# Performance work log

Measured on AMD Instinct MI355X. Metric: run time of the kernel, lower is better.

## Reference

```python
import jax, jax.numpy as jnp
import numpy as np

EMBED_DIM = 512

def setup_inputs() -> dict:
    key = jax.random.key(0)
    ks = jax.random.split(key, 8)
    B, N, M, C = 4, 4096, 4096, EMBED_DIM
    s = 1.0 / np.sqrt(C)
    return {
        "rgb_features": jax.random.normal(ks[0], (B, N, C), jnp.float32),
        "depth_features": jax.random.normal(ks[1], (B, M, C), jnp.float32),
        "Wq": jax.random.normal(ks[2], (C, C), jnp.float32) * s,
        "bq": jnp.zeros((C,), jnp.float32),
        "Wk": jax.random.normal(ks[3], (C, C), jnp.float32) * s,
        "bk": jnp.zeros((C,), jnp.float32),
        "Wv": jax.random.normal(ks[4], (C, C), jnp.float32) * s,
        "bv": jnp.zeros((C,), jnp.float32),
    }

def reference(rgb_features, depth_features, Wq, bq, Wk, bk, Wv, bv):
    C = rgb_features.shape[-1]
    scale = C ** (-0.5)
    Q = rgb_features @ Wq + bq          # [B, N, C]
    K = depth_features @ Wk + bk        # [B, M, C]
    V = depth_features @ Wv + bv        # [B, M, C]
    scores = jnp.einsum('bnc,bmc->bnm', Q, K) * scale
    attn = jax.nn.softmax(scores, axis=-1)
    return jnp.einsum('bnm,bmc->bnc', attn, V)
```

## Files before the change

kernel.cpp:

```cpp
#include <hip/hip_runtime.h>
#include <hip/hip_bf16.h>
#include <stdint.h>


typedef unsigned short u16;
typedef __attribute__((ext_vector_type(8))) short bf16x8;
typedef __attribute__((ext_vector_type(16))) float f32x16;
typedef __attribute__((ext_vector_type(4))) unsigned short u16x4;

#define GLD_LDS16(g, l)                                                        \
  __builtin_amdgcn_global_load_lds(                                            \
      (const __attribute__((address_space(1))) unsigned int*)(g),              \
      (__attribute__((address_space(3))) unsigned int*)(l), 16, 0, 0)

__device__ __forceinline__ u16 f2bf(float f) {
  unsigned x = __float_as_uint(f);
  return (u16)((x + 0x7fffu + ((x >> 16) & 1u)) >> 16);
}

template <int TM, int TN, int WC, int BIAS_MODE, bool OUT_F32, bool SCALE_EN,
          int MINW>
__global__ __launch_bounds__(256, MINW) void gemm32(
    const u16* __restrict__ A, const u16* __restrict__ Bm,
    const float* __restrict__ bias, void* __restrict__ Cv, int M, int N, int K,
    long long sAb, long long sBb, long long sCb, float scale) {
  constexpr int WROWS = TM * WC / 4;
  constexpr int WCOLS = TN / WC;
  constexpr int MSUB = WROWS / 32;
  constexpr int NSUB = WCOLS / 32;
  constexpr int CA = TM / 64;
  constexpr int CB = TN / 64;

  const int bz = blockIdx.z;
  A += (size_t)bz * sAb;
  Bm += (size_t)bz * sBb;

  const int bm = blockIdx.y * TM;
  const int bn = blockIdx.x * TN;

  __shared__ u16 As[TM * 32];
  __shared__ u16 Bs[TN * 32];

  const int tid = threadIdx.x;
  const int wave = tid >> 6;
  const int lane = tid & 63;
  const int ln31 = lane & 31;
  const int half = lane >> 5;
  const int wr = wave / WC;
  const int wc = wave % WC;

  const int rowA = lane >> 2;
  const int swz = ((lane & 3) ^ ((rowA + (rowA >> 2)) & 3)) * 8;
  const int gl = (ln31 + (ln31 >> 2)) & 3;

  f32x16 acc[MSUB][NSUB] = {};

  for (int k0 = 0; k0 < K; k0 += 32) {
    __syncthreads();
#pragma unroll
    for (int r = 0; r < CA; ++r) {
      const int ch = wave * CA + r;
      GLD_LDS16(A + (size_t)(bm + ch * 16 + rowA) * K + k0 + swz,
                As + ch * 16 * 32);
    }
#pragma unroll
    for (int r = 0; r < CB; ++r) {
      const int ch = wave * CB + r;
      GLD_LDS16(Bm + (size_t)(bn + ch * 16 + rowA) * K + k0 + swz,
                Bs + ch * 16 * 32);
    }
    __syncthreads();

#pragma unroll
    for (int kc = 0; kc < 2; ++kc) {
      const int p = ((kc * 2 + half) ^ gl) * 8;
      bf16x8 af[MSUB], bfv[NSUB];
#pragma unroll
      for (int mt = 0; mt < MSUB; ++mt)
        af[mt] = *(const bf16x8*)&As[(wr * WROWS + mt * 32 + ln31) * 32 + p];
#pragma unroll
      for (int nt = 0; nt < NSUB; ++nt)
        bfv[nt] = *(const bf16x8*)&Bs[(wc * WCOLS + nt * 32 + ln31) * 32 + p];
#pragma unroll
      for (int mt = 0; mt < MSUB; ++mt)
#pragma unroll
        for (int nt = 0; nt < NSUB; ++nt)
          acc[mt][nt] = __builtin_amdgcn_mfma_f32_32x32x16_bf16(
              af[mt], bfv[nt], acc[mt][nt], 0, 0, 0);
    }
  }

  const int crow0 = bm + wr * WROWS + 4 * half;
  const int ccol0 = bn + wc * WCOLS + ln31;
#pragma unroll
  for (int mt = 0; mt < MSUB; ++mt) {
#pragma unroll
    for (int nt = 0; nt < NSUB; ++nt) {
      const int col = ccol0 + nt * 32;
#pragma unroll
      for (int r = 0; r < 16; ++r) {
        const int row = crow0 + mt * 32 + (r & 3) + 8 * (r >> 2);
        float v = acc[mt][nt][r];
        if constexpr (SCALE_EN) v *= scale;
        if constexpr (BIAS_MODE == 1) v += bias[col];
        if constexpr (BIAS_MODE == 2) v += bias[row];
        const size_t idx = (size_t)bz * (size_t)sCb + (size_t)row * N + col;
        if constexpr (OUT_F32)
          ((float*)Cv)[idx] = v;
        else
          ((u16*)Cv)[idx] = f2bf(v);
      }
    }
  }
}

__global__ __launch_bounds__(256) void cvt_pair(const float* __restrict__ x,
                                                const float* __restrict__ y,
                                                u16* __restrict__ ox,
                                                u16* __restrict__ oy, int n4) {
  const int i = blockIdx.x * 256 + threadIdx.x;
  if (i >= n4) return;
  const float4 a = ((const float4*)x)[i];
  const float4 b = ((const float4*)y)[i];
  u16x4 oa, ob;
  oa[0] = f2bf(a.x); oa[1] = f2bf(a.y); oa[2] = f2bf(a.z); oa[3] = f2bf(a.w);
  ob[0] = f2bf(b.x); ob[1] = f2bf(b.y); ob[2] = f2bf(b.z); ob[3] = f2bf(b.w);
  ((u16x4*)ox)[i] = oa;
  ((u16x4*)oy)[i] = ob;
}

__global__ __launch_bounds__(256) void wtrans_k(const float* __restrict__ W,
                                                u16* __restrict__ WT) {
  const int tr = blockIdx.y * 64;
  const int tc = blockIdx.x * 64;
  __shared__ float T[64][65];
  const int t = threadIdx.x;
  const int r0 = t >> 4;
  const int c0 = (t & 15) * 4;
#pragma unroll
  for (int rr = 0; rr < 4; ++rr) {
    const int row = rr * 16 + r0;
    const float4 w = *(const float4*)&W[(size_t)(tr + row) * 512 + tc + c0];
    T[row][c0 + 0] = w.x; T[row][c0 + 1] = w.y;
    T[row][c0 + 2] = w.z; T[row][c0 + 3] = w.w;
  }
  __syncthreads();
#pragma unroll
  for (int rr = 0; rr < 4; ++rr) {
    const int orow = rr * 16 + r0;
    u16x4 o;
#pragma unroll
    for (int j = 0; j < 4; ++j) o[j] = f2bf(T[c0 + j][orow]);
    *(u16x4*)&WT[(size_t)(tc + orow) * 512 + tr + c0] = o;
  }
}

__global__ __launch_bounds__(256) void softmax_rows(u16* __restrict__ S,
                                                    int cols) {
  u16* p = S + (size_t)blockIdx.x * (size_t)cols;
  const int tid = threadIdx.x;
  const int lane = tid & 63;
  const int wave = tid >> 6;

  uint4 d[2];
  d[0] = ((const uint4*)p)[tid];
  d[1] = ((const uint4*)p)[tid + 256];

  float v[16];
#pragma unroll
  for (int i = 0; i < 2; ++i) {
    const unsigned* w = (const unsigned*)&d[i];
#pragma unroll
    for (int j = 0; j < 4; ++j) {
      v[i * 8 + j * 2 + 0] = __uint_as_float(w[j] << 16);
      v[i * 8 + j * 2 + 1] = __uint_as_float(w[j] & 0xffff0000u);
    }
  }

  float mx = -3.4e38f;
#pragma unroll
  for (int i = 0; i < 16; ++i) mx = fmaxf(mx, v[i]);
#pragma unroll
  for (int o = 32; o > 0; o >>= 1) mx = fmaxf(mx, __shfl_xor(mx, o, 64));

  __shared__ float red[4];
  if (lane == 0) red[wave] = mx;
  __syncthreads();
  mx = fmaxf(fmaxf(red[0], red[1]), fmaxf(red[2], red[3]));

  float s = 0.f;
#pragma unroll
  for (int i = 0; i < 16; ++i) {
    v[i] = __expf(v[i] - mx);
    s += v[i];
  }
#pragma unroll
  for (int o = 32; o > 0; o >>= 1) s += __shfl_xor(s, o, 64);
  __syncthreads();
  if (lane == 0) red[wave] = s;
  __syncthreads();
  s = (red[0] + red[1]) + (red[2] + red[3]);
  const float inv = 1.0f / s;

  uint4 o4[2];
#pragma unroll
  for (int i = 0; i < 2; ++i) {
    unsigned* w = (unsigned*)&o4[i];
#pragma unroll
    for (int j = 0; j < 4; ++j) {
      const unsigned lo = f2bf(v[i * 8 + j * 2 + 0] * inv);
      const unsigned hi = f2bf(v[i * 8 + j * 2 + 1] * inv);
      w[j] = lo | (hi << 16);
    }
  }
  ((uint4*)p)[tid] = o4[0];
  ((uint4*)p)[tid + 256] = o4[1];
}

extern "C" void kernel_launch(void* const* d_in, const int* in_sizes, int n_in,
                              void* d_out, int out_size, void* d_ws,
                              size_t ws_size, hipStream_t stream) {
  const float* rgb = (const float*)d_in[0];
  const float* dep = (const float*)d_in[1];
  const float* Wq = (const float*)d_in[2];
  const float* bq = (const float*)d_in[3];
  const float* Wk = (const float*)d_in[4];
  const float* bk = (const float*)d_in[5];
  const float* Wv = (const float*)d_in[6];
  const float* bv = (const float*)d_in[7];
  float* out = (float*)d_out;

  const int B = 4, N = 4096, M = 4096, C = 512;
  const size_t nBNC = (size_t)B * N * C;
  const float scale = 0.044194173824159216f;

  char* ws = (char*)d_ws;
  size_t off = 0;
  auto carve = [&](size_t bytes) -> void* {
    void* p = ws + off;
    off += (bytes + 255) & ~(size_t)255;
    return p;
  };
  u16* rgb_bf = (u16*)carve(nBNC * 2);
  u16* dep_bf = (u16*)carve(nBNC * 2);
  u16* WqT = (u16*)carve((size_t)C * C * 2);
  u16* WkT = (u16*)carve((size_t)C * C * 2);
  u16* WvT = (u16*)carve((size_t)C * C * 2);
  u16* Qb = (u16*)carve(nBNC * 2);
  u16* Kb = (u16*)carve(nBNC * 2);
  u16* Vt = (u16*)carve(nBNC * 2);
  const size_t base = off;
  const size_t sFull = (size_t)B * N * M * 2;
  const size_t sOne = (size_t)N * M * 2;
  const bool full = ws_size >= base + sFull;
  u16* Sb = (u16*)carve(full ? sFull : sOne);

  cvt_pair<<<8192, 256, 0, stream>>>(rgb, dep, rgb_bf, dep_bf, (int)(nBNC / 4));
  wtrans_k<<<dim3(8, 8), 256, 0, stream>>>(Wq, WqT);
  wtrans_k<<<dim3(8, 8), 256, 0, stream>>>(Wk, WkT);
  wtrans_k<<<dim3(8, 8), 256, 0, stream>>>(Wv, WvT);

  const long long strQ = (long long)N * C;
  const long long strS = (long long)N * M;
  const long long strV = (long long)C * M;

  gemm32<128, 128, 2, 1, false, false, 4><<<dim3(4, 128, 1), 256, 0, stream>>>(
      rgb_bf, WqT, bq, Qb, 16384, 512, 512, 0, 0, 0, 1.f);
  gemm32<128, 128, 2, 1, false, false, 4><<<dim3(4, 128, 1), 256, 0, stream>>>(
      dep_bf, WkT, bk, Kb, 16384, 512, 512, 0, 0, 0, 1.f);
  gemm32<128, 128, 2, 2, false, false, 4><<<dim3(32, 4, 4), 256, 0, stream>>>(
      WvT, dep_bf, bv, Vt, 512, 4096, 512, 0, strQ, strV, 1.f);

  if (full) {
    gemm32<256, 128, 2, 0, false, true, 2><<<dim3(32, 16, 4), 256, 0, stream>>>(
        Qb, Kb, nullptr, Sb, 4096, 4096, 512, strQ, strQ, strS, scale);
    softmax_rows<<<16384, 256, 0, stream>>>(Sb, 4096);
    gemm32<64, 256, 4, 0, true, false, 4><<<dim3(2, 64, 4), 256, 0, stream>>>(
        Sb, Vt, nullptr, out, 4096, 512, 4096, strS, strV, strQ, 1.f);
  } else {
    for (int b = 0; b < 4; ++b) {
      gemm32<256, 128, 2, 0, false, true, 2>
          <<<dim3(32, 16, 1), 256, 0, stream>>>(Qb + (size_t)b * strQ,
                                                Kb + (size_t)b * strQ, nullptr,
                                                Sb, 4096, 4096, 512, 0, 0, 0,
                                                scale);
      softmax_rows<<<4096, 256, 0, stream>>>(Sb, 4096);
      gemm32<64, 256, 4, 0, true, false, 4><<<dim3(2, 64, 1), 256, 0, stream>>>(
          Sb, Vt + (size_t)b * strV, nullptr, out + (size_t)b * strQ, 4096, 512,
          4096, 0, 0, 0, 1.f);
    }
  }
}
```

Before: 415.0 us.

## Fuse exp and row-sum into QK GEMM epilogue, normalize in new PV kernel

Drops the separate softmax pass. The QK^T GEMM epilogue now writes exp(scaled score) as bf16 and atomically accumulates per-row denominators into a zeroed buffer. A new double-buffered 512-thread PV GEMM divides its output by the denominator at the end. This removes a full read and write of the B×N×M score matrix. It skips max subtraction, which risks overflow for large scores. It also drops the per-batch fallback for small workspaces and adds atomic contention on the denominators.

```diff
diff --git a/kernel.cpp b/kernel.cpp
--- a/kernel.cpp
+++ b/kernel.cpp
@@ -19,11 +19,12 @@
 }
 
 template <int TM, int TN, int WC, int BIAS_MODE, bool OUT_F32, bool SCALE_EN,
-          int MINW>
+          int MINW, bool EXPDEN>
 __global__ __launch_bounds__(256, MINW) void gemm32(
     const u16* __restrict__ A, const u16* __restrict__ Bm,
-    const float* __restrict__ bias, void* __restrict__ Cv, int M, int N, int K,
-    long long sAb, long long sBb, long long sCb, float scale) {
+    const float* __restrict__ bias, void* __restrict__ Cv,
+    float* __restrict__ den, int M, int N, int K, long long sAb, long long sBb,
+    long long sCb, float scale) {
   constexpr int WROWS = TM * WC / 4;
   constexpr int WCOLS = TN / WC;
   constexpr int MSUB = WROWS / 32;
@@ -92,26 +93,150 @@
 
   const int crow0 = bm + wr * WROWS + 4 * half;
   const int ccol0 = bn + wc * WCOLS + ln31;
-#pragma unroll
-  for (int mt = 0; mt < MSUB; ++mt) {
-#pragma unroll
-    for (int nt = 0; nt < NSUB; ++nt) {
-      const int col = ccol0 + nt * 32;
+
+  if constexpr (EXPDEN) {
+    float rsum[MSUB][16];
+#pragma unroll
+    for (int mt = 0; mt < MSUB; ++mt)
+#pragma unroll
+      for (int r = 0; r < 16; ++r) rsum[mt][r] = 0.f;
+#pragma unroll
+    for (int mt = 0; mt < MSUB; ++mt) {
+#pragma unroll
+      for (int nt = 0; nt < NSUB; ++nt) {
+        const int col = ccol0 + nt * 32;
+#pragma unroll
+        for (int r = 0; r < 16; ++r) {
+          const int row = crow0 + mt * 32 + (r & 3) + 8 * (r >> 2);
+          const float e = __expf(acc[mt][nt][r] * scale);
+          ((u16*)Cv)[(size_t)bz * (size_t)sCb + (size_t)row * N + col] =
+              f2bf(e);
+          rsum[mt][r] += e;
+        }
+      }
+    }
+#pragma unroll
+    for (int mt = 0; mt < MSUB; ++mt) {
 #pragma unroll
       for (int r = 0; r < 16; ++r) {
-        const int row = crow0 + mt * 32 + (r & 3) + 8 * (r >> 2);
-        float v = acc[mt][nt][r];
-        if constexpr (SCALE_EN) v *= scale;
-        if constexpr (BIAS_MODE == 1) v += bias[col];
-        if constexpr (BIAS_MODE == 2) v += bias[row];
-        const size_t idx = (size_t)bz * (size_t)sCb + (size_t)row * N + col;
-        if constexpr (OUT_F32)
-          ((float*)Cv)[idx] = v;
-        else
-          ((u16*)Cv)[idx] = f2bf(v);
+        float s = rsum[mt][r];
+        s += __shfl_xor(s, 1, 64);
+        s += __shfl_xor(s, 2, 64);
+        s += __shfl_xor(s, 4, 64);
+        s += __shfl_xor(s, 8, 64);
+        s += __shfl_xor(s, 16, 64);
+        if (ln31 == 0) {
+          const int row = crow0 + mt * 32 + (r & 3) + 8 * (r >> 2);
+          atomicAdd(&den[bz * M + row], s);
+        }
       }
     }
-  }
+  } else {
+#pragma unroll
+    for (int mt = 0; mt < MSUB; ++mt) {
+#pragma unroll
+      for (int nt = 0; nt < NSUB; ++nt) {
+        const int col = ccol0 + nt * 32;
+#pragma unroll
+        for (int r = 0; r < 16; ++r) {
+          const int row = crow0 + mt * 32 + (r & 3) + 8 * (r >> 2);
+          float v = acc[mt][nt][r];
+          if constexpr (SCALE_EN) v *= scale;
+          if constexpr (BIAS_MODE == 1) v += bias[col];
+          if constexpr (BIAS_MODE == 2) v += bias[row];
+          const size_t idx = (size_t)bz * (size_t)sCb + (size_t)row * N + col;
+          if constexpr (OUT_F32)
+            ((float*)Cv)[idx] = v;
+          else
+            ((u16*)Cv)[idx] = f2bf(v);
+        }
+      }
+    }
+  }
+}
+
+__global__ __launch_bounds__(512, 2) void pv_gemm(
+    const u16* __restrict__ P, const u16* __restrict__ Vt,
+    const float* __restrict__ den, float* __restrict__ O) {
+  const int bz = blockIdx.z;
+  const u16* A = P + (size_t)bz * (4096ull * 4096ull);
+  const u16* B = Vt + (size_t)bz * (512ull * 4096ull);
+  float* Ob = O + (size_t)bz * (4096ull * 512ull);
+  const float* dn = den + bz * 4096;
+
+  const int bm = blockIdx.y * 128;
+  const int bn = blockIdx.x * 256;
+
+  __shared__ u16 As[2][128 * 32];
+  __shared__ u16 Bs[2][256 * 32];
+
+  const int tid = threadIdx.x;
+  const int wave = tid >> 6;
+  const int lane = tid & 63;
+  const int ln31 = lane & 31;
+  const int half = lane >> 5;
+  const int wr = wave >> 2;
+  const int wc = wave & 3;
+
+  const int rowA = lane >> 2;
+  const int swz = ((lane & 3) ^ ((rowA + (rowA >> 2)) & 3)) * 8;
+  const int gl = (ln31 + (ln31 >> 2)) & 3;
+
+  f32x16 acc[2][2] = {};
+
+  auto stage = [&](int buf, int k0) {
+    GLD_LDS16(A + (size_t)(bm + wave * 16 + rowA) * 4096 + k0 + swz,
+              As[buf] + wave * 16 * 32);
+#pragma unroll
+    for (int r = 0; r < 2; ++r) {
+      const int ch = wave * 2 + r;
+      GLD_LDS16(B + (size_t)(bn + ch * 16 + rowA) * 4096 + k0 + swz,
+                Bs[buf] + ch * 16 * 32);
+    }
+  };
+
+  stage(0, 0);
+  for (int it = 0; it < 128; ++it) {
+    __syncthreads();
+    if (it + 1 < 128) stage((it + 1) & 1, (it + 1) * 32);
+    const int buf = it & 1;
+#pragma unroll
+    for (int kc = 0; kc < 2; ++kc) {
+      const int p = ((kc * 2 + half) ^ gl) * 8;
+      bf16x8 af[2], bfv[2];
+#pragma unroll
+      for (int mt = 0; mt < 2; ++mt)
+        af[mt] = *(const bf16x8*)&As[buf][(wr * 64 + mt * 32 + ln31) * 32 + p];
+#pragma unroll
+      for (int nt = 0; nt < 2; ++nt)
+        bfv[nt] = *(const bf16x8*)&Bs[buf][(wc * 64 + nt * 32 + ln31) * 32 + p];
+#pragma unroll
+      for (int mt = 0; mt < 2; ++mt)
+#pragma unroll
+        for (int nt = 0; nt < 2; ++nt)
+          acc[mt][nt] = __builtin_amdgcn_mfma_f32_32x32x16_bf16(
+              af[mt], bfv[nt], acc[mt][nt], 0, 0, 0);
+    }
+  }
+
+  const int crow0 = bm + wr * 64 + 4 * half;
+  const int ccol0 = bn + wc * 64 + ln31;
+#pragma unroll
+  for (int mt = 0; mt < 2; ++mt) {
+#pragma unroll
+    for (int r = 0; r < 16; ++r) {
+      const int row = crow0 + mt * 32 + (r & 3) + 8 * (r >> 2);
+      const float rd = 1.0f / dn[row];
+#pragma unroll
+      for (int nt = 0; nt < 2; ++nt)
+        Ob[(size_t)row * 512 + ccol0 + nt * 32] = acc[mt][nt][r] * rd;
+    }
+  }
+}
+
+__global__ __launch_bounds__(256) void zero_f32(float* __restrict__ p, int n) {
+  const int i = blockIdx.x * 256 + threadIdx.x;
+  if (i < n) p[i] = 0.f;
 }
 
 __global__ __launch_bounds__(256) void cvt_pair(const float* __restrict__ x,
@@ -153,68 +278,6 @@
     for (int j = 0; j < 4; ++j) o[j] = f2bf(T[c0 + j][orow]);
     *(u16x4*)&WT[(size_t)(tc + orow) * 512 + tr + c0] = o;
   }
-}
-
-__global__ __launch_bounds__(256) void softmax_rows(u16* __restrict__ S,
-                                                    int cols) {
-  u16* p = S + (size_t)blockIdx.x * (size_t)cols;
-  const int tid = threadIdx.x;
-  const int lane = tid & 63;
-  const int wave = tid >> 6;
-
-  uint4 d[2];
-  d[0] = ((const uint4*)p)[tid];
-  d[1] = ((const uint4*)p)[tid + 256];
-
-  float v[16];
-#pragma unroll
-  for (int i = 0; i < 2; ++i) {
-    const unsigned* w = (const unsigned*)&d[i];
-#pragma unroll
-    for (int j = 0; j < 4; ++j) {
-      v[i * 8 + j * 2 + 0] = __uint_as_float(w[j] << 16);
-      v[i * 8 + j * 2 + 1] = __uint_as_float(w[j] & 0xffff0000u);
-    }
-  }
-
-  float mx = -3.4e38f;
-#pragma unroll
-  for (int i = 0; i < 16; ++i) mx = fmaxf(mx, v[i]);
-#pragma unroll
-  for (int o = 32; o > 0; o >>= 1) mx = fmaxf(mx, __shfl_xor(mx, o, 64));
-
-  __shared__ float red[4];
-  if (lane == 0) red[wave] = mx;
-  __syncthreads();
-  mx = fmaxf(fmaxf(red[0], red[1]), fmaxf(red[2], red[3]));
-
-  float s = 0.f;
-#pragma unroll
-  for (int i = 0; i < 16; ++i) {
-    v[i] = __expf(v[i] - mx);
-    s += v[i];
-  }
-#pragma unroll
-  for (int o = 32; o > 0; o >>= 1) s += __shfl_xor(s, o, 64);
-  __syncthreads();
-  if (lane == 0) red[wave] = s;
-  __syncthreads();
-  s = (red[0] + red[1]) + (red[2] + red[3]);
-  const float inv = 1.0f / s;
-
-  uint4 o4[2];
-#pragma unroll
-  for (int i = 0; i < 2; ++i) {
-    unsigned* w = (unsigned*)&o4[i];
-#pragma unroll
-    for (int j = 0; j < 4; ++j) {
-      const unsigned lo = f2bf(v[i * 8 + j * 2 + 0] * inv);
-      const unsigned hi = f2bf(v[i * 8 + j * 2 + 1] * inv);
-      w[j] = lo | (hi << 16);
-    }
-  }
-  ((uint4*)p)[tid] = o4[0];
-  ((uint4*)p)[tid + 256] = o4[1];
 }
 
 extern "C" void kernel_launch(void* const* d_in, const int* in_sizes, int n_in,
@@ -249,45 +312,32 @@
   u16* Qb = (u16*)carve(nBNC * 2);
   u16* Kb = (u16*)carve(nBNC * 2);
   u16* Vt = (u16*)carve(nBNC * 2);
-  const size_t base = off;
-  const size_t sFull = (size_t)B * N * M * 2;
-  const size_t sOne = (size_t)N * M * 2;
-  const bool full = ws_size >= base + sFull;
-  u16* Sb = (u16*)carve(full ? sFull : sOne);
+  float* den = (float*)carve((size_t)B * N * 4);
+  u16* Sb = (u16*)carve((size_t)B * N * M * 2);
+
+  const long long strQ = (long long)N * C;
+  const long long strS = (long long)N * M;
+  const long long strV = (long long)C * M;
 
   cvt_pair<<<8192, 256, 0, stream>>>(rgb, dep, rgb_bf, dep_bf, (int)(nBNC / 4));
   wtrans_k<<<dim3(8, 8), 256, 0, stream>>>(Wq, WqT);
   wtrans_k<<<dim3(8, 8), 256, 0, stream>>>(Wk, WkT);
   wtrans_k<<<dim3(8, 8), 256, 0, stream>>>(Wv, WvT);
-
-  const long long strQ = (long long)N * C;
-  const long long strS = (long long)N * M;
-  const long long strV = (long long)C * M;
-
-  gemm32<128, 128, 2, 1, false, false, 4><<<dim3(4, 128, 1), 256, 0, stream>>>(
-      rgb_bf, WqT, bq, Qb, 16384, 512, 512, 0, 0, 0, 1.f);
-  gemm32<128, 128, 2, 1, false, false, 4><<<dim3(4, 128, 1), 256, 0, stream>>>(
-      dep_bf, WkT, bk, Kb, 16384, 512, 512, 0, 0, 0, 1.f);
-  gemm32<128, 128, 2, 2, false, false, 4><<<dim3(32, 4, 4), 256, 0, stream>>>(
-      WvT, dep_bf, bv, Vt, 512, 4096, 512, 0, strQ, strV, 1.f);
-
-  if (full) {
-    gemm32<256, 128, 2, 0, false, true, 2><<<dim3(32, 16, 4), 256, 0, stream>>>(
-        Qb, Kb, nullptr, Sb, 4096, 4096, 512, strQ, strQ, strS, scale);
-    softmax_rows<<<16384, 256, 0, stream>>>(Sb, 4096);
-    gemm32<64, 256, 4, 0, true, false, 4><<<dim3(2, 64, 4), 256, 0, stream>>>(
-        Sb, Vt, nullptr, out, 4096, 512, 4096, strS, strV, strQ, 1.f);
-  } else {
-    for (int b = 0; b < 4; ++b) {
-      gemm32<256, 128, 2, 0, false, true, 2>
-          <<<dim3(32, 16, 1), 256, 0, stream>>>(Qb + (size_t)b * strQ,
-                                                Kb + (size_t)b * strQ, nullptr,
-                                                Sb, 4096, 4096, 512, 0, 0, 0,
-                                                scale);
-      softmax_rows<<<4096, 256, 0, stream>>>(Sb, 4096);
-      gemm32<64, 256, 4, 0, true, false, 4><<<dim3(2, 64, 1), 256, 0, stream>>>(
-          Sb, Vt + (size_t)b * strV, nullptr, out + (size_t)b * strQ, 4096, 512,
-          4096, 0, 0, 0, 1.f);
-    }
-  }
-}
+  zero_f32<<<64, 256, 0, stream>>>(den, B * N);
+
+  gemm32<128, 128, 2, 1, false, false, 4, false>
+      <<<dim3(4, 128, 1), 256, 0, stream>>>(rgb_bf, WqT, bq, Qb, nullptr, 16384,
+                                            512, 512, 0, 0, 0, 1.f);
+  gemm32<128, 128, 2, 1, false, false, 4, false>
+      <<<dim3(4, 128, 1), 256, 0, stream>>>(dep_bf, WkT, bk, Kb, nullptr, 16384,
+                                            512, 512, 0, 0, 0, 1.f);
+  gemm32<128, 128, 2, 2, false, false, 4, false>
+      <<<dim3(32, 4, 4), 256, 0, stream>>>(WvT, dep_bf, bv, Vt, nullptr, 512,
+                                           4096, 512, 0, strQ, strV, 1.f);
+
+  gemm32<256, 128, 2, 0, false, true, 2, true>
+      <<<dim3(32, 16, 4), 256, 0, stream>>>(Qb, Kb, nullptr, Sb, den, 4096,
+                                            4096, 512, strQ, strQ, strS, scale);
+
+  pv_gemm<<<dim3(2, 32, 4), 512, 0, stream>>>(Sb, Vt, den, out);
+}
```

After: 476.8 us. +14.9%, slower.
